# Optimization experiments

Hardware: AMD Instinct MI355X
Metric: run time of the kernel (lower is better)

Reference implementation:

```python
import jax, jax.numpy as jnp
import numpy as np

N_NODES = 50000
N_EDGES = 800000
IN_CH, HID_CH, OUT_CH = 128, 256, 128
BN_EPS = 1e-5


def gcn_conv(x, W, b, src, dst):
    """PyG GCNConv: h = x @ W; symmetric normalization with self-loops; scatter-add; + bias."""
    N = x.shape[0]
    h = x @ W  # [N, out_ch]
    # degree including self-loop (all edge weights = 1)
    deg = jax.ops.segment_sum(jnp.ones(src.shape[0], h.dtype), dst, num_segments=N) + 1.0
    dis = jax.lax.rsqrt(deg)  # deg^-1/2
    norm = dis[src] * dis[dst]  # [E]
    agg = jax.ops.segment_sum(h[src] * norm[:, None], dst, num_segments=N)
    # self-loop contribution: norm_ii = dis[i]^2
    return agg + h * (dis * dis)[:, None] + b


def batchnorm_train(x, gamma, beta):
    mu = jnp.mean(x, axis=0)
    var = jnp.mean((x - mu) ** 2, axis=0)  # biased var, as torch BN uses for normalization
    return (x - mu) * jax.lax.rsqrt(var + BN_EPS) * gamma + beta


def setup_inputs() -> dict:
    key = jax.random.key(0)
    ks = jax.random.split(key, 4)
    x = jax.random.normal(ks[0], (N_NODES, IN_CH), dtype=jnp.float32)
    edge_index = jax.random.randint(ks[1], (2, N_EDGES), 0, N_NODES, dtype=jnp.int64 if jax.config.jax_enable_x64 else jnp.int32)
    W1 = jax.random.normal(ks[2], (IN_CH, HID_CH), dtype=jnp.float32) * (1.0 / np.sqrt(IN_CH))
    W2 = jax.random.normal(ks[3], (HID_CH, OUT_CH), dtype=jnp.float32) * (1.0 / np.sqrt(HID_CH))
    return {
        "x": x,
        "edge_index": edge_index,
        "W1": W1,
        "b1": jnp.zeros((HID_CH,), jnp.float32),
        "gamma1": jnp.ones((HID_CH,), jnp.float32),
        "beta1": jnp.zeros((HID_CH,), jnp.float32),
        "W2": W2,
        "b2": jnp.zeros((OUT_CH,), jnp.float32),
    }


def reference(x, edge_index, W1, b1, gamma1, beta1, W2, b2):
    src, dst = edge_index[0], edge_index[1]
    h = gcn_conv(x, W1, b1, src, dst)
    h = jax.nn.relu(batchnorm_train(h, gamma1, beta1))
    # dropout omitted (deterministic eval-style reference)
    return gcn_conv(h, W2, b2, src, dst)
```

## Files before the change

### kernel.cpp

```cpp
#include <hip/hip_runtime.h>

#define N_NODES 50000
#define N_EDGES 800000
#define C_IN 128
#define C_HID 256
#define C_OUT 128
#define BN_EPS 1e-5f

typedef __bf16 v8bf __attribute__((ext_vector_type(8)));
typedef float f32x4 __attribute__((ext_vector_type(4)));
typedef unsigned short u16x8 __attribute__((ext_vector_type(8)));

static __device__ __forceinline__ unsigned short f2bf(float f) {
    unsigned int u = __float_as_uint(f);
    u += 0x7fffu + ((u >> 16) & 1u);
    return (unsigned short)(u >> 16);
}
static __device__ __forceinline__ float bf2f(unsigned short h) {
    return __uint_as_float((unsigned int)h << 16);
}
static __device__ __forceinline__ unsigned int pack2(float a, float b) {
    return (unsigned int)f2bf(a) | ((unsigned int)f2bf(b) << 16);
}
static __device__ __forceinline__ float lo2f(unsigned int u) { return __uint_as_float(u << 16); }
static __device__ __forceinline__ float hi2f(unsigned int u) { return __uint_as_float(u & 0xffff0000u); }

#define DEG_BLOCKS ((N_EDGES + 255) / 256)
#define CAST_BLOCKS ((N_NODES * 16 + 255) / 256)


__global__ __launch_bounds__(256) void k_deg_wtrans(const int* __restrict__ dst, int* __restrict__ deg4,
                                                    int* __restrict__ rank,
                                                    const float* __restrict__ W1, const float* __restrict__ W2,
                                                    unsigned short* __restrict__ WT1, unsigned short* __restrict__ WT2,
                                                    const float* __restrict__ x, unsigned short* __restrict__ xb) {
    int bx = blockIdx.x, t = threadIdx.x;
    if (bx < DEG_BLOCKS) {
        int e = bx * 256 + t;
        if (e < N_EDGES) {
            int s = e & 3;
            rank[e] = atomicAdd(&deg4[s * N_NODES + dst[e]], 1);
        }
    } else if (bx < DEG_BLOCKS + 256) {
        int i = (bx - DEG_BLOCKS) * 256 + t;
        if (i < C_IN * C_HID) {
            int n = i >> 7, k = i & 127;
            WT1[n * C_IN + k] = f2bf(W1[k * C_HID + n]);
        } else {
            int j = i - C_IN * C_HID;
            int n = j >> 8, k = j & 255;
            WT2[n * C_HID + k] = f2bf(W2[k * C_OUT + n]);
        }
    } else {
        int i = (bx - DEG_BLOCKS - 256) * 256 + t;
        int node = i >> 4;
        if (node < N_NODES) {
            int g8 = (i & 15) * 8;
            float4 v0 = *(const float4*)&x[(size_t)node * C_IN + g8];
            float4 v1 = *(const float4*)&x[(size_t)node * C_IN + g8 + 4];
            uint4 o = make_uint4(pack2(v0.x, v0.y), pack2(v0.z, v0.w),
                                 pack2(v1.x, v1.y), pack2(v1.z, v1.w));
            *(uint4*)&xb[(size_t)node * C_IN + g8] = o;
        }
    }
}


__global__ __launch_bounds__(512) void k_scan1(int* __restrict__ deg4, int* __restrict__ rs,
                                               int* __restrict__ partial, float* __restrict__ dis) {
    __shared__ int s[512];
    int t = threadIdx.x;
    int i = blockIdx.x * 512 + t;
    int v = 0;
    if (i < N_NODES) {
        int d0 = deg4[i];
        int d1 = deg4[N_NODES + i];
        int d2 = deg4[2 * N_NODES + i];
        int d3 = deg4[3 * N_NODES + i];
        v = d0 + d1 + d2 + d3;
        deg4[N_NODES + i] = d0;
        deg4[2 * N_NODES + i] = d0 + d1;
        deg4[3 * N_NODES + i] = d0 + d1 + d2;
        dis[i] = rsqrtf((float)v + 1.0f);
    }
    s[t] = v;
    __syncthreads();
    for (int off = 1; off < 512; off <<= 1) {
        int tv = (t >= off) ? s[t - off] : 0;
        __syncthreads();
        s[t] += tv;
        __syncthreads();
    }
    if (i < N_NODES) rs[i + 1] = s[t];
    if (t == 511) partial[blockIdx.x] = s[511];
}

__global__ __launch_bounds__(256) void k_scan23(int* __restrict__ rs, const int* __restrict__ partial,
                                                int nb) {
    __shared__ int pre[128];
    __shared__ int wsum[2];
    int t = threadIdx.x;
    int lane = t & 63;
    int pv = 0, v = 0;
    if (t < 128) {
        pv = (t < nb) ? partial[t] : 0;
        v = pv;
#pragma unroll
        for (int off = 1; off < 64; off <<= 1) {
            int u = __shfl_up(v, off);
            if (lane >= off) v += u;
        }
        if (lane == 63) wsum[t >> 6] = v;
    }
    __syncthreads();
    if (t < 128) {
        if (t >= 64) v += wsum[0];
        pre[t] = v - pv;
    }
    __syncthreads();
    int i = blockIdx.x * 256 + t;
    if (i < N_NODES) {
        rs[i + 1] = rs[i + 1] + pre[i >> 9];
    }
    if (i == 0) rs[0] = 0;
}


#define PLACE_BLOCKS ((N_EDGES / 4 + 255) / 256)

__global__ __launch_bounds__(256) void k_place(const int* __restrict__ src, const int* __restrict__ dst,
                                               const int* __restrict__ rank, const int* __restrict__ rs,
                                               const int* __restrict__ deg4, int* __restrict__ eidx) {
    int q = blockIdx.x * 256 + threadIdx.x;
    int e = q * 4;
    if (e < N_EDGES) {
        int4 d4 = *(const int4*)&dst[e];
        int4 r4 = *(const int4*)&rank[e];
        int4 s4 = *(const int4*)&src[e];
        eidx[rs[d4.x] + r4.x] = s4.x;
        eidx[rs[d4.y] + deg4[N_NODES + d4.y] + r4.y] = s4.y;
        eidx[rs[d4.z] + deg4[2 * N_NODES + d4.z] + r4.z] = s4.z;
        eidx[rs[d4.w] + deg4[3 * N_NODES + d4.w] + r4.w] = s4.w;
    }
}


template <bool FINAL>
__global__ __launch_bounds__(256) void k_aggr(const unsigned short* __restrict__ g,
                                              const float* __restrict__ dis, const float* __restrict__ bias,
                                              const int* __restrict__ rs, const int* __restrict__ eidx,
                                              unsigned short* __restrict__ outb, float* __restrict__ outf) {
    int wid = (blockIdx.x * 256 + threadIdx.x) >> 6;
    int lane = threadIdx.x & 63;
    if (wid >= N_NODES) return;
    int slot = lane >> 4;
    int cp = lane & 15;
    int s = rs[wid], e = rs[wid + 1];
    float a0 = 0.f, a1 = 0.f, a2 = 0.f, a3 = 0.f, a4 = 0.f, a5 = 0.f, a6 = 0.f, a7 = 0.f;
    int p = s;
    for (; p + 15 < e; p += 16) {
        int i0 = eidx[p + slot];
        int i1 = eidx[p + 4 + slot];
        int i2 = eidx[p + 8 + slot];
        int i3 = eidx[p + 12 + slot];
        u16x8 v0 = *(const u16x8*)&g[(size_t)i0 * 128 + cp * 8];
        u16x8 v1 = *(const u16x8*)&g[(size_t)i1 * 128 + cp * 8];
        u16x8 v2 = *(const u16x8*)&g[(size_t)i2 * 128 + cp * 8];
        u16x8 v3 = *(const u16x8*)&g[(size_t)i3 * 128 + cp * 8];
        if (FINAL) {
            a0 += bf2f(v0[0]) + bf2f(v1[0]) + bf2f(v2[0]) + bf2f(v3[0]);
            a1 += bf2f(v0[1]) + bf2f(v1[1]) + bf2f(v2[1]) + bf2f(v3[1]);
            a2 += bf2f(v0[2]) + bf2f(v1[2]) + bf2f(v2[2]) + bf2f(v3[2]);
            a3 += bf2f(v0[3]) + bf2f(v1[3]) + bf2f(v2[3]) + bf2f(v3[3]);
            a4 += bf2f(v0[4]) + bf2f(v1[4]) + bf2f(v2[4]) + bf2f(v3[4]);
            a5 += bf2f(v0[5]) + bf2f(v1[5]) + bf2f(v2[5]) + bf2f(v3[5]);
            a6 += bf2f(v0[6]) + bf2f(v1[6]) + bf2f(v2[6]) + bf2f(v3[6]);
            a7 += bf2f(v0[7]) + bf2f(v1[7]) + bf2f(v2[7]) + bf2f(v3[7]);
        } else {
            float w0 = dis[i0], w1 = dis[i1], w2 = dis[i2], w3 = dis[i3];
            a0 = fmaf(w0, bf2f(v0[0]), fmaf(w1, bf2f(v1[0]), fmaf(w2, bf2f(v2[0]), fmaf(w3, bf2f(v3[0]), a0))));
            a1 = fmaf(w0, bf2f(v0[1]), fmaf(w1, bf2f(v1[1]), fmaf(w2, bf2f(v2[1]), fmaf(w3, bf2f(v3[1]), a1))));
            a2 = fmaf(w0, bf2f(v0[2]), fmaf(w1, bf2f(v1[2]), fmaf(w2, bf2f(v2[2]), fmaf(w3, bf2f(v3[2]), a2))));
            a3 = fmaf(w0, bf2f(v0[3]), fmaf(w1, bf2f(v1[3]), fmaf(w2, bf2f(v2[3]), fmaf(w3, bf2f(v3[3]), a3))));
            a4 = fmaf(w0, bf2f(v0[4]), fmaf(w1, bf2f(v1[4]), fmaf(w2, bf2f(v2[4]), fmaf(w3, bf2f(v3[4]), a4))));
            a5 = fmaf(w0, bf2f(v0[5]), fmaf(w1, bf2f(v1[5]), fmaf(w2, bf2f(v2[5]), fmaf(w3, bf2f(v3[5]), a5))));
            a6 = fmaf(w0, bf2f(v0[6]), fmaf(w1, bf2f(v1[6]), fmaf(w2, bf2f(v2[6]), fmaf(w3, bf2f(v3[6]), a6))));
            a7 = fmaf(w0, bf2f(v0[7]), fmaf(w1, bf2f(v1[7]), fmaf(w2, bf2f(v2[7]), fmaf(w3, bf2f(v3[7]), a7))));
        }
    }
    if (p < e) {
        int last = e - 1;
        int j0 = p + slot;
        int j1 = j0 + 4;
        int j2 = j0 + 8;
        int j3 = j0 + 12;
        float m0 = (j0 <= last) ? 1.f : 0.f;
        float m1 = (j1 <= last) ? 1.f : 0.f;
        float m2 = (j2 <= last) ? 1.f : 0.f;
        float m3 = (j3 <= last) ? 1.f : 0.f;
        j0 = min(j0, last); j1 = min(j1, last); j2 = min(j2, last); j3 = min(j3, last);
        int i0 = eidx[j0];
        int i1 = eidx[j1];
        int i2 = eidx[j2];
        int i3 = eidx[j3];
        float w0 = m0, w1 = m1, w2 = m2, w3 = m3;
        if (!FINAL) {
            w0 = m0 * dis[i0]; w1 = m1 * dis[i1]; w2 = m2 * dis[i2]; w3 = m3 * dis[i3];
        }
        u16x8 v0 = *(const u16x8*)&g[(size_t)i0 * 128 + cp * 8];
        u16x8 v1 = *(const u16x8*)&g[(size_t)i1 * 128 + cp * 8];
        u16x8 v2 = *(const u16x8*)&g[(size_t)i2 * 128 + cp * 8];
        u16x8 v3 = *(const u16x8*)&g[(size_t)i3 * 128 + cp * 8];
        a0 = fmaf(w0, bf2f(v0[0]), fmaf(w1, bf2f(v1[0]), fmaf(w2, bf2f(v2[0]), fmaf(w3, bf2f(v3[0]), a0))));
        a1 = fmaf(w0, bf2f(v0[1]), fmaf(w1, bf2f(v1[1]), fmaf(w2, bf2f(v2[1]), fmaf(w3, bf2f(v3[1]), a1))));
        a2 = fmaf(w0, bf2f(v0[2]), fmaf(w1, bf2f(v1[2]), fmaf(w2, bf2f(v2[2]), fmaf(w3, bf2f(v3[2]), a2))));
        a3 = fmaf(w0, bf2f(v0[3]), fmaf(w1, bf2f(v1[3]), fmaf(w2, bf2f(v2[3]), fmaf(w3, bf2f(v3[3]), a3))));
        a4 = fmaf(w0, bf2f(v0[4]), fmaf(w1, bf2f(v1[4]), fmaf(w2, bf2f(v2[4]), fmaf(w3, bf2f(v3[4]), a4))));
        a5 = fmaf(w0, bf2f(v0[5]), fmaf(w1, bf2f(v1[5]), fmaf(w2, bf2f(v2[5]), fmaf(w3, bf2f(v3[5]), a5))));
        a6 = fmaf(w0, bf2f(v0[6]), fmaf(w1, bf2f(v1[6]), fmaf(w2, bf2f(v2[6]), fmaf(w3, bf2f(v3[6]), a6))));
        a7 = fmaf(w0, bf2f(v0[7]), fmaf(w1, bf2f(v1[7]), fmaf(w2, bf2f(v2[7]), fmaf(w3, bf2f(v3[7]), a7))));
    }
    a0 += __shfl_xor(a0, 16); a1 += __shfl_xor(a1, 16); a2 += __shfl_xor(a2, 16); a3 += __shfl_xor(a3, 16);
    a4 += __shfl_xor(a4, 16); a5 += __shfl_xor(a5, 16); a6 += __shfl_xor(a6, 16); a7 += __shfl_xor(a7, 16);
    a0 += __shfl_xor(a0, 32); a1 += __shfl_xor(a1, 32); a2 += __shfl_xor(a2, 32); a3 += __shfl_xor(a3, 32);
    a4 += __shfl_xor(a4, 32); a5 += __shfl_xor(a5, 32); a6 += __shfl_xor(a6, 32); a7 += __shfl_xor(a7, 32);
    if (slot < 2) {
        int ch = cp * 8 + slot * 4;
        float r0 = slot ? a4 : a0, r1 = slot ? a5 : a1, r2 = slot ? a6 : a2, r3 = slot ? a7 : a3;
        ushort4 gi = *(const ushort4*)&g[(size_t)wid * 128 + ch];
        float d = dis[wid];
        if (FINAL) {
            float4 bv = *(const float4*)&bias[ch];
            float4 o = make_float4(fmaf(d, r0 + bf2f(gi.x), bv.x), fmaf(d, r1 + bf2f(gi.y), bv.y),
                                   fmaf(d, r2 + bf2f(gi.z), bv.z), fmaf(d, r3 + bf2f(gi.w), bv.w));
            *(float4*)&outf[(size_t)wid * 128 + ch] = o;
        } else {
            float d2 = d * d;
            ushort4 z;
            z.x = f2bf(fmaf(d, r0, d2 * bf2f(gi.x)));
            z.y = f2bf(fmaf(d, r1, d2 * bf2f(gi.y)));
            z.z = f2bf(fmaf(d, r2, d2 * bf2f(gi.z)));
            z.w = f2bf(fmaf(d, r3, d2 * bf2f(gi.w)));
            *(ushort4*)&outb[(size_t)wid * 128 + ch] = z;
        }
    }
}


template <bool TRANS, int KC>
__global__ __launch_bounds__(256, 2) void k_gemmv(const unsigned short* __restrict__ Ah,
                                                  const unsigned short* __restrict__ BT,
                                                  unsigned short* __restrict__ C,
                                                  const float* __restrict__ dis, const float* __restrict__ bias,
                                                  float* __restrict__ bnsum, float* __restrict__ bnsq,
                                                  const float* __restrict__ gamma, const float* __restrict__ beta,
                                                  int M, int N) {
    constexpr int K = KC * 32;
    constexpr int BP = K + 8;
    __shared__ unsigned short Blds[64 * BP];
    __shared__ float tsc_s[K];
    __shared__ float tof_s[K];

    int t = threadIdx.x;
    int w = t >> 6, lane = t & 63;
    int lm = lane & 15, quad = lane >> 4;
    int col0 = blockIdx.y * 64;

    if (TRANS && t < K) {
        float inv_n = 1.0f / (float)N_NODES;
        float mu = bnsum[t] * inv_n;
        float var = bnsq[t] * inv_n - mu * mu;
        float a = gamma[t] * rsqrtf(var + BN_EPS);
        tsc_s[t] = a;
        tof_s[t] = beta[t] - mu * a;
    }
    constexpr int NLD = 64 * K / 8;
    for (int j = t; j < NLD; j += 256) {
        int n = j / (K / 8);
        int kq = j % (K / 8);
        *(uint4*)&Blds[n * BP + kq * 8] = *(const uint4*)&BT[(size_t)(col0 + n) * K + kq * 8];
    }
    __syncthreads();
    v8bf bfr[4][KC];
#pragma unroll
    for (int in = 0; in < 4; ++in)
#pragma unroll
        for (int kc = 0; kc < KC; ++kc)
            bfr[in][kc] = *(const v8bf*)&Blds[(in * 16 + lm) * BP + kc * 32 + quad * 8];
    __syncthreads();

    unsigned short* Ct = Blds + w * (16 * 80);

    float bias_r[4];
    if (!TRANS) {
#pragma unroll
        for (int in = 0; in < 4; ++in) bias_r[in] = bias[col0 + in * 16 + lm];
    }
    float ss[4] = {0.f, 0.f, 0.f, 0.f}, qq[4] = {0.f, 0.f, 0.f, 0.f};

    int strip0 = (blockIdx.x * 4 + w) * 4;
#pragma unroll
    for (int s = 0; s < 4; ++s) {
        int strip = strip0 + s;
        if (strip * 16 >= M) break;
        int arow = strip * 16 + lm;
        uint4 araw[KC];
#pragma unroll
        for (int kc = 0; kc < KC; ++kc)
            araw[kc] = *(const uint4*)&Ah[(size_t)arow * K + kc * 32 + quad * 8];
        float dqa[4];
        if (TRANS) *(float4*)dqa = *(const float4*)&dis[strip * 16 + quad * 4];
        f32x4 acc[4] = {};
#pragma unroll
        for (int kc = 0; kc < KC; ++kc) {
            v8bf af;
            if (TRANS) {
                int kb2 = kc * 32 + quad * 8;
                float4 s0 = *(const float4*)&tsc_s[kb2];
                float4 s1 = *(const float4*)&tsc_s[kb2 + 4];
                float4 o0 = *(const float4*)&tof_s[kb2];
                float4 o1 = *(const float4*)&tof_s[kb2 + 4];
                uint4 h = araw[kc];
                float f0 = fmaxf(fmaf(lo2f(h.x), s0.x, o0.x), 0.f);
                float f1 = fmaxf(fmaf(hi2f(h.x), s0.y, o0.y), 0.f);
                float f2 = fmaxf(fmaf(lo2f(h.y), s0.z, o0.z), 0.f);
                float f3 = fmaxf(fmaf(hi2f(h.y), s0.w, o0.w), 0.f);
                float f4 = fmaxf(fmaf(lo2f(h.z), s1.x, o1.x), 0.f);
                float f5 = fmaxf(fmaf(hi2f(h.z), s1.y, o1.y), 0.f);
                float f6 = fmaxf(fmaf(lo2f(h.w), s1.z, o1.z), 0.f);
                float f7 = fmaxf(fmaf(hi2f(h.w), s1.w, o1.w), 0.f);
                uint4 pk = make_uint4(pack2(f0, f1), pack2(f2, f3), pack2(f4, f5), pack2(f6, f7));
                af = *(v8bf*)&pk;
            } else {
                af = *(v8bf*)&araw[kc];
            }
#pragma unroll
            for (int in = 0; in < 4; ++in)
                acc[in] = __builtin_amdgcn_mfma_f32_16x16x32_bf16(af, bfr[in][kc], acc[in], 0, 0, 0);
        }
#pragma unroll
        for (int in = 0; in < 4; ++in) {
#pragma unroll
            for (int q = 0; q < 4; ++q) {
                float val = TRANS ? acc[in][q] * dqa[q] : acc[in][q] + bias_r[in];
                unsigned short hb = f2bf(val);
                Ct[(quad * 4 + q) * 80 + in * 16 + lm] = hb;
                if (!TRANS) {
                    float v = bf2f(hb);
                    ss[in] += v;
                    qq[in] = fmaf(v, v, qq[in]);
                }
            }
        }
#pragma unroll
        for (int it = 0; it < 2; ++it) {
            int rl = (lane >> 3) + it * 8;
            uint4 v = *(const uint4*)&Ct[rl * 80 + (lane & 7) * 8];
            *(uint4*)&C[(size_t)(strip * 16 + rl) * N + col0 + (lane & 7) * 8] = v;
        }
    }
    if (!TRANS) {
#pragma unroll
        for (int in = 0; in < 4; ++in) {
            float s = ss[in], q2 = qq[in];
            s += __shfl_xor(s, 16); q2 += __shfl_xor(q2, 16);
            s += __shfl_xor(s, 32); q2 += __shfl_xor(q2, 32);
            if (quad == 0) {
                atomicAdd(&bnsum[col0 + in * 16 + lm], s);
                atomicAdd(&bnsq[col0 + in * 16 + lm], q2);
            }
        }
    }
}


extern "C" void kernel_launch(void* const* d_in, const int* in_sizes, int n_in,
                              void* d_out, int out_size, void* d_ws, size_t ws_size,
                              hipStream_t stream) {
    const float* x      = (const float*)d_in[0];
    const int*   ei     = (const int*)d_in[1];
    const float* W1     = (const float*)d_in[2];
    const float* b1     = (const float*)d_in[3];
    const float* gamma1 = (const float*)d_in[4];
    const float* beta1  = (const float*)d_in[5];
    const float* W2     = (const float*)d_in[6];
    const float* b2     = (const float*)d_in[7];
    const int* srcv = ei;
    const int* dstv = ei + N_EDGES;
    float* out = (float*)d_out;

    char* w = (char*)d_ws;
    size_t off = 0;
    auto alloc = [&](size_t bytes) {
        void* p = w + off;
        off = (off + bytes + 255) & ~(size_t)255;
        return p;
    };
    int*   deg4    = (int*)alloc((size_t)N_NODES * 4 * 4);
    float* bnsum   = (float*)alloc(256 * 4);
    float* bnsq    = (float*)alloc(256 * 4);
    size_t zero_bytes = off;
    float* dis     = (float*)alloc(N_NODES * 4);
    int*   rs      = (int*)alloc((N_NODES + 1) * 4);
    int*   rank    = (int*)alloc((size_t)N_EDGES * 4);
    int*   partial = (int*)alloc(128 * 4);
    int*   eidx    = (int*)alloc((size_t)N_EDGES * 4);
    unsigned short* WT1 = (unsigned short*)alloc((size_t)C_IN * C_HID * 2);
    unsigned short* WT2 = (unsigned short*)alloc((size_t)C_HID * C_OUT * 2);
    unsigned short* xb  = (unsigned short*)alloc((size_t)N_NODES * C_IN * 2);
    unsigned short* P   = (unsigned short*)alloc((size_t)N_NODES * C_IN * 2);
    unsigned short* z1  = (unsigned short*)alloc((size_t)N_NODES * C_HID * 2);
    unsigned short* g2  = (unsigned short*)alloc((size_t)N_NODES * C_OUT * 2);
    (void)ws_size; (void)in_sizes; (void)n_in; (void)out_size;

    (void)hipMemsetAsync(deg4, 0, zero_bytes, stream);

    int nb = (N_NODES + 511) / 512;
    k_deg_wtrans<<<DEG_BLOCKS + 256 + CAST_BLOCKS, 256, 0, stream>>>(dstv, deg4, rank, W1, W2, WT1, WT2,
                                                                     x, xb);
    k_scan1<<<nb, 512, 0, stream>>>(deg4, rs, partial, dis);
    k_scan23<<<(N_NODES + 255) / 256, 256, 0, stream>>>(rs, partial, nb);
    k_place<<<PLACE_BLOCKS, 256, 0, stream>>>(srcv, dstv, rank, rs, deg4, eidx);

    k_aggr<false><<<(N_NODES * 64 + 255) / 256, 256, 0, stream>>>(xb, dis, nullptr, rs, eidx, P, nullptr);
    dim3 gg1((N_NODES + 255) / 256, C_HID / 64);
    k_gemmv<false, 4><<<gg1, 256, 0, stream>>>(P, WT1, z1, nullptr, b1, bnsum, bnsq, nullptr, nullptr,
                                               N_NODES, C_HID);

    dim3 gg2((N_NODES + 255) / 256, C_OUT / 64);
    k_gemmv<true, 8><<<gg2, 256, 0, stream>>>(z1, WT2, g2, dis, nullptr, bnsum, bnsq, gamma1, beta1,
                                              N_NODES, C_OUT);
    k_aggr<true><<<(N_NODES * 64 + 255) / 256, 256, 0, stream>>>(g2, dis, b2, rs, eidx, nullptr, out);
}
```

Baseline: 250.0 us.

## Compute all output columns per block in GEMM to read A rows once

The GEMM kernels now cover the full output width in each block instead of splitting columns across a second grid dimension. Each block loads the whole transposed weight into LDS and reads B fragments from LDS per MFMA rather than holding them in registers. The intent is to read each A row, and apply the BN/ReLU transform on it, only once instead of once per 64-column slice. The cost is larger LDS use per block, extra LDS reads inside the inner loop, and a grid of 196 blocks, which may leave some CUs idle.

Result: slower. 256.2 us (+2.5%).

```diff
diff --git a/kernel.cpp b/kernel.cpp
--- a/kernel.cpp
+++ b/kernel.cpp
@@ -247,24 +247,25 @@
 }
 
 
-template <bool TRANS, int KC>
+template <bool TRANS, int KC, int NP>
 __global__ __launch_bounds__(256, 2) void k_gemmv(const unsigned short* __restrict__ Ah,
                                                   const unsigned short* __restrict__ BT,
                                                   unsigned short* __restrict__ C,
                                                   const float* __restrict__ dis, const float* __restrict__ bias,
                                                   float* __restrict__ bnsum, float* __restrict__ bnsq,
                                                   const float* __restrict__ gamma, const float* __restrict__ beta,
-                                                  int M, int N) {
+                                                  int M) {
     constexpr int K = KC * 32;
+    constexpr int N = NP * 64;
     constexpr int BP = K + 8;
-    __shared__ unsigned short Blds[64 * BP];
+    __shared__ unsigned short Blds[N * BP];
+    __shared__ unsigned short Cts[4 * 16 * 80];
     __shared__ float tsc_s[K];
     __shared__ float tof_s[K];
 
     int t = threadIdx.x;
     int w = t >> 6, lane = t & 63;
     int lm = lane & 15, quad = lane >> 4;
-    int col0 = blockIdx.y * 64;
 
     if (TRANS && t < K) {
         float inv_n = 1.0f / (float)N_NODES;
@@ -274,29 +275,24 @@
         tsc_s[t] = a;
         tof_s[t] = beta[t] - mu * a;
     }
-    constexpr int NLD = 64 * K / 8;
+    constexpr int NLD = N * K / 8;
     for (int j = t; j < NLD; j += 256) {
         int n = j / (K / 8);
         int kq = j % (K / 8);
-        *(uint4*)&Blds[n * BP + kq * 8] = *(const uint4*)&BT[(size_t)(col0 + n) * K + kq * 8];
+        *(uint4*)&Blds[n * BP + kq * 8] = *(const uint4*)&BT[(size_t)n * K + kq * 8];
     }
     __syncthreads();
-    v8bf bfr[4][KC];
-#pragma unroll
-    for (int in = 0; in < 4; ++in)
-#pragma unroll
-        for (int kc = 0; kc < KC; ++kc)
-            bfr[in][kc] = *(const v8bf*)&Blds[(in * 16 + lm) * BP + kc * 32 + quad * 8];
-    __syncthreads();
-
-    unsigned short* Ct = Blds + w * (16 * 80);
-
-    float bias_r[4];
+
+    unsigned short* Ct = Cts + w * (16 * 80);
+
+    float bias_r[NP][4];
     if (!TRANS) {
 #pragma unroll
-        for (int in = 0; in < 4; ++in) bias_r[in] = bias[col0 + in * 16 + lm];
-    }
-    float ss[4] = {0.f, 0.f, 0.f, 0.f}, qq[4] = {0.f, 0.f, 0.f, 0.f};
+        for (int p = 0; p < NP; ++p)
+#pragma unroll
+            for (int in = 0; in < 4; ++in) bias_r[p][in] = bias[p * 64 + in * 16 + lm];
+    }
+    float ss[NP][4] = {}, qq[NP][4] = {};
 
     int strip0 = (blockIdx.x * 4 + w) * 4;
 #pragma unroll
@@ -304,23 +300,16 @@
         int strip = strip0 + s;
         if (strip * 16 >= M) break;
         int arow = strip * 16 + lm;
-        uint4 araw[KC];
-#pragma unroll
-        for (int kc = 0; kc < KC; ++kc)
-            araw[kc] = *(const uint4*)&Ah[(size_t)arow * K + kc * 32 + quad * 8];
-        float dqa[4];
-        if (TRANS) *(float4*)dqa = *(const float4*)&dis[strip * 16 + quad * 4];
-        f32x4 acc[4] = {};
+        v8bf afr[KC];
 #pragma unroll
         for (int kc = 0; kc < KC; ++kc) {
-            v8bf af;
+            uint4 h = *(const uint4*)&Ah[(size_t)arow * K + kc * 32 + quad * 8];
             if (TRANS) {
                 int kb2 = kc * 32 + quad * 8;
                 float4 s0 = *(const float4*)&tsc_s[kb2];
                 float4 s1 = *(const float4*)&tsc_s[kb2 + 4];
                 float4 o0 = *(const float4*)&tof_s[kb2];
                 float4 o1 = *(const float4*)&tof_s[kb2 + 4];
-                uint4 h = araw[kc];
                 float f0 = fmaxf(fmaf(lo2f(h.x), s0.x, o0.x), 0.f);
                 float f1 = fmaxf(fmaf(hi2f(h.x), s0.y, o0.y), 0.f);
                 float f2 = fmaxf(fmaf(lo2f(h.y), s0.z, o0.z), 0.f);
@@ -330,46 +319,59 @@
                 float f6 = fmaxf(fmaf(lo2f(h.w), s1.z, o1.z), 0.f);
                 float f7 = fmaxf(fmaf(hi2f(h.w), s1.w, o1.w), 0.f);
                 uint4 pk = make_uint4(pack2(f0, f1), pack2(f2, f3), pack2(f4, f5), pack2(f6, f7));
-                af = *(v8bf*)&pk;
+                afr[kc] = *(v8bf*)&pk;
             } else {
-                af = *(v8bf*)&araw[kc];
+                afr[kc] = *(v8bf*)&h;
             }
-#pragma unroll
-            for (int in = 0; in < 4; ++in)
-                acc[in] = __builtin_amdgcn_mfma_f32_16x16x32_bf16(af, bfr[in][kc], acc[in], 0, 0, 0);
-        }
-#pragma unroll
-        for (int in = 0; in < 4; ++in) {
-#pragma unroll
-            for (int q = 0; q < 4; ++q) {
-                float val = TRANS ? acc[in][q] * dqa[q] : acc[in][q] + bias_r[in];
-                unsigned short hb = f2bf(val);
-                Ct[(quad * 4 + q) * 80 + in * 16 + lm] = hb;
-                if (!TRANS) {
-                    float v = bf2f(hb);
-                    ss[in] += v;
-                    qq[in] = fmaf(v, v, qq[in]);
+        }
+        float dqa[4];
+        if (TRANS) *(float4*)dqa = *(const float4*)&dis[strip * 16 + quad * 4];
+#pragma unroll
+        for (int p = 0; p < NP; ++p) {
+            f32x4 acc[4] = {};
+#pragma unroll
+            for (int kc = 0; kc < KC; ++kc) {
+#pragma unroll
+                for (int in = 0; in < 4; ++in) {
+                    v8bf bf = *(const v8bf*)&Blds[(p * 64 + in * 16 + lm) * BP + kc * 32 + quad * 8];
+                    acc[in] = __builtin_amdgcn_mfma_f32_16x16x32_bf16(afr[kc], bf, acc[in], 0, 0, 0);
                 }
             }
-        }
-#pragma unroll
-        for (int it = 0; it < 2; ++it) {
-            int rl = (lane >> 3) + it * 8;
-            uint4 v = *(const uint4*)&Ct[rl * 80 + (lane & 7) * 8];
-            *(uint4*)&C[(size_t)(strip * 16 + rl) * N + col0 + (lane & 7) * 8] = v;
+#pragma unroll
+            for (int in = 0; in < 4; ++in) {
+#pragma unroll
+                for (int q = 0; q < 4; ++q) {
+                    float val = TRANS ? acc[in][q] * dqa[q] : acc[in][q] + bias_r[p][in];
+                    unsigned short hb = f2bf(val);
+                    Ct[(quad * 4 + q) * 80 + in * 16 + lm] = hb;
+                    if (!TRANS) {
+                        float v = bf2f(hb);
+                        ss[p][in] += v;
+                        qq[p][in] = fmaf(v, v, qq[p][in]);
+                    }
+                }
+            }
+#pragma unroll
+            for (int it = 0; it < 2; ++it) {
+                int rl = (lane >> 3) + it * 8;
+                uint4 v = *(const uint4*)&Ct[rl * 80 + (lane & 7) * 8];
+                *(uint4*)&C[(size_t)(strip * 16 + rl) * N + p * 64 + (lane & 7) * 8] = v;
+            }
         }
     }
     if (!TRANS) {
 #pragma unroll
-        for (int in = 0; in < 4; ++in) {
-            float s = ss[in], q2 = qq[in];
-            s += __shfl_xor(s, 16); q2 += __shfl_xor(q2, 16);
-            s += __shfl_xor(s, 32); q2 += __shfl_xor(q2, 32);
-            if (quad == 0) {
-                atomicAdd(&bnsum[col0 + in * 16 + lm], s);
-                atomicAdd(&bnsq[col0 + in * 16 + lm], q2);
+        for (int p = 0; p < NP; ++p)
+#pragma unroll
+            for (int in = 0; in < 4; ++in) {
+                float s = ss[p][in], q2 = qq[p][in];
+                s += __shfl_xor(s, 16); q2 += __shfl_xor(q2, 16);
+                s += __shfl_xor(s, 32); q2 += __shfl_xor(q2, 32);
+                if (quad == 0) {
+                    atomicAdd(&bnsum[p * 64 + in * 16 + lm], s);
+                    atomicAdd(&bnsq[p * 64 + in * 16 + lm], q2);
+                }
             }
-        }
     }
 }
 
@@ -423,12 +425,10 @@
     k_place<<<PLACE_BLOCKS, 256, 0, stream>>>(srcv, dstv, rank, rs, deg4, eidx);
 
     k_aggr<false><<<(N_NODES * 64 + 255) / 256, 256, 0, stream>>>(xb, dis, nullptr, rs, eidx, P, nullptr);
-    dim3 gg1((N_NODES + 255) / 256, C_HID / 64);
-    k_gemmv<false, 4><<<gg1, 256, 0, stream>>>(P, WT1, z1, nullptr, b1, bnsum, bnsq, nullptr, nullptr,
-                                               N_NODES, C_HID);
-
-    dim3 gg2((N_NODES + 255) / 256, C_OUT / 64);
-    k_gemmv<true, 8><<<gg2, 256, 0, stream>>>(z1, WT2, g2, dis, nullptr, bnsum, bnsq, gamma1, beta1,
-                                              N_NODES, C_OUT);
+    k_gemmv<false, 4, 4><<<196, 256, 0, stream>>>(P, WT1, z1, nullptr, b1, bnsum, bnsq, nullptr, nullptr,
+                                                  N_NODES);
+
+    k_gemmv<true, 8, 2><<<196, 256, 0, stream>>>(z1, WT2, g2, dis, nullptr, bnsum, bnsq, gamma1, beta1,
+                                                 N_NODES);
     k_aggr<true><<<(N_NODES * 64 + 255) / 256, 256, 0, stream>>>(g2, dis, b2, rs, eidx, nullptr, out);
 }
```
